# Optimization experiments

Measured on AMD Instinct MI355X. Metric: run time of the kernel, lower is better.

Reference implementation:

```python
import jax, jax.numpy as jnp
import numpy as np

D_MODEL = 2048
D_LATENT = 512


def setup_inputs() -> dict:
    key = jax.random.key(0)
    ks = jax.random.split(key, 6)
    x = jax.random.normal(ks[0], (2, 4096, D_MODEL), dtype=jnp.float32)
    cache = jax.random.normal(ks[1], (2, 4096, D_LATENT), dtype=jnp.float32)
    s = 0.02
    # weights stored (in_features, out_features); equivalent to torch Linear (no bias)
    W_kv = jax.random.normal(ks[2], (D_MODEL, D_LATENT), dtype=jnp.float32) * s
    W_q = jax.random.normal(ks[3], (D_MODEL, D_MODEL), dtype=jnp.float32) * s
    W_lq = jax.random.normal(ks[4], (D_MODEL, D_LATENT), dtype=jnp.float32) * s
    W_o = jax.random.normal(ks[5], (D_LATENT, D_MODEL), dtype=jnp.float32) * s
    return {"x": x, "cache": cache, "W_kv": W_kv, "W_q": W_q, "W_lq": W_lq, "W_o": W_o}


def reference(x, cache, W_kv, W_q, W_lq, W_o):
    # latent compression of inputs: (B, S, d_latent)
    l_kv_new = jnp.einsum('bsd,dl->bsl', x, W_kv)
    # query path: x -> query (d_model) -> latent query (d_latent)
    q = jnp.einsum('bsd,de->bse', x, W_q)
    lq = jnp.einsum('bse,el->bsl', q, W_lq)
    # append to cache: (B, T+S, d_latent)
    l_kv = jnp.concatenate([cache, l_kv_new], axis=1)
    scale = jnp.sqrt(jnp.float32(D_LATENT)).astype(x.dtype)
    # attention in latent space: scores (B, S, T+S)
    scores = jnp.einsum('bsl,btl->bst', lq, l_kv) / scale
    weights = jax.nn.softmax(scores, axis=-1)
    ctx = jnp.einsum('bst,btl->bsl', weights, l_kv)
    out = jnp.einsum('bsl,ld->bsd', ctx, W_o)
    return out, l_kv
```

## Files before the change

kernel.cpp:

```cpp
#include <hip/hip_runtime.h>
#include <hip/hip_bf16.h>
#include <math.h>


typedef _Float16 f16x8 __attribute__((ext_vector_type(8)));
typedef _Float16 f16x4 __attribute__((ext_vector_type(4)));
typedef float    f32x4 __attribute__((ext_vector_type(4)));
typedef float    f32x8 __attribute__((ext_vector_type(8)));


__global__ __launch_bounds__(256) void k_cvt(const float* __restrict__ in,
                                             _Float16* __restrict__ out, int n4) {
  int i = blockIdx.x * blockDim.x + threadIdx.x;
  int st = gridDim.x * blockDim.x;
  for (; i < n4; i += st) {
    f32x4 v = reinterpret_cast<const f32x4*>(in)[i];
    reinterpret_cast<f16x4*>(out)[i] = __builtin_convertvector(v, f16x4);
  }
}

__global__ __launch_bounds__(256) void k_cache(const float* __restrict__ cache,
                                               float* __restrict__ lkv_f32,
                                               _Float16* __restrict__ lkv16, int n4) {
  int i = blockIdx.x * blockDim.x + threadIdx.x;
  int st = gridDim.x * blockDim.x;
  for (; i < n4; i += st) {
    f32x4 v = reinterpret_cast<const f32x4*>(cache)[i];
    int e = i << 2;
    int b = e >> 21;
    int dst = e + (b << 21);
    *reinterpret_cast<f32x4*>(lkv_f32 + dst) = v;
    *reinterpret_cast<f16x4*>(lkv16 + dst) = __builtin_convertvector(v, f16x4);
  }
}

__global__ __launch_bounds__(256) void k_tc(const float* __restrict__ in,
                                            _Float16* __restrict__ out, int R, int C) {
  __shared__ float t[32][33];
  const int c0 = blockIdx.x << 5, r0 = blockIdx.y << 5;
  const int tid = threadIdx.x;
  {
    int r = tid >> 3, c4 = (tid & 7) << 2;
    f32x4 v = *reinterpret_cast<const f32x4*>(&in[(long)(r0 + r) * C + c0 + c4]);
    t[r][c4] = v[0]; t[r][c4 + 1] = v[1]; t[r][c4 + 2] = v[2]; t[r][c4 + 3] = v[3];
  }
  __syncthreads();
  {
    int c = tid >> 3, r4 = (tid & 7) << 2;
    f16x4 o = {(_Float16)t[r4][c], (_Float16)t[r4 + 1][c],
               (_Float16)t[r4 + 2][c], (_Float16)t[r4 + 3][c]};
    *reinterpret_cast<f16x4*>(&out[(long)(c0 + c) * R + r0 + r4]) = o;
  }
}

__global__ __launch_bounds__(256) void k_tb(const _Float16* __restrict__ in,
                                            _Float16* __restrict__ out, int R, int C) {
  __shared__ _Float16 t[32][36];
  const int c0 = blockIdx.x << 5, r0 = blockIdx.y << 5;
  const int tid = threadIdx.x;
  {
    int r = tid >> 3, c4 = (tid & 7) << 2;
    f16x4 v = *reinterpret_cast<const f16x4*>(&in[(long)(r0 + r) * C + c0 + c4]);
    t[r][c4] = v[0]; t[r][c4 + 1] = v[1]; t[r][c4 + 2] = v[2]; t[r][c4 + 3] = v[3];
  }
  __syncthreads();
  {
    int c = tid >> 3, r4 = (tid & 7) << 2;
    f16x4 o = {t[r4][c], t[r4 + 1][c], t[r4 + 2][c], t[r4 + 3][c]};
    *reinterpret_cast<f16x4*>(&out[(long)(c0 + c) * R + r0 + r4]) = o;
  }
}

template <int CMODE>
__global__ __launch_bounds__(256) void k_gemm(const _Float16* __restrict__ A,
                                              const _Float16* __restrict__ B,
                                              float* __restrict__ Cf,
                                              _Float16* __restrict__ Ch,
                                              int M, int N, int K, int lda, int ldb,
                                              float cscale) {
  if constexpr (CMODE == 4) {
    const long z = blockIdx.z;
    A += z * K;
    B += z * K;
    Cf += z * (long)M * N;
  }
  __shared__ alignas(16) _Float16 As[128 * 64];
  __shared__ alignas(16) _Float16 Bs[128 * 64];
  const int tid = threadIdx.x;
  const int lane = tid & 63;
  const int w = tid >> 6;
  const int wr = ((w >> 1) & 1) << 6, wc = (w & 1) << 6;
  const int bm = blockIdx.x << 7, bn = blockIdx.y << 7;
  const int g = lane >> 4, ln15 = lane & 15;

  f32x4 acc[4][4] = {};

  const int srowl = lane >> 3;
  const int skcol = (lane & 7) << 3;
  const int wofs = (srowl << 6) + (((lane & 7) ^ srowl) << 3);

  f16x8 ra[4], rb[4];
  auto loadregs = [&](int k0) {
#pragma unroll
    for (int i = 0; i < 4; ++i) {
      int ch = (w << 2) + i;
      int row = (ch << 3) + srowl;
      ra[i] = *reinterpret_cast<const f16x8*>(&A[(long)(bm + row) * lda + k0 + skcol]);
      rb[i] = *reinterpret_cast<const f16x8*>(&B[(long)(bn + row) * ldb + k0 + skcol]);
    }
  };
  loadregs(0);
  const int nk = K >> 6;
  for (int kt = 0; kt < nk; ++kt) {
    __syncthreads();
#pragma unroll
    for (int i = 0; i < 4; ++i) {
      int ch = (w << 2) + i;
      *reinterpret_cast<f16x8*>(&As[(ch << 9) + wofs]) = ra[i];
      *reinterpret_cast<f16x8*>(&Bs[(ch << 9) + wofs]) = rb[i];
    }
    __syncthreads();
    if (kt + 1 < nk) loadregs((kt + 1) << 6);
#pragma unroll
    for (int ks = 0; ks < 2; ++ks) {
      f16x8 af[4], bf[4];
#pragma unroll
      for (int i = 0; i < 4; ++i) {
        const int arow = wr + (i << 4) + ln15;
        const int brow = wc + (i << 4) + ln15;
        const int inner = (((ks << 5) + (g << 3)) ^ ((ln15 & 7) << 3));
        af[i] = *reinterpret_cast<const f16x8*>(&As[arow * 64 + inner]);
        bf[i] = *reinterpret_cast<const f16x8*>(&Bs[brow * 64 + inner]);
      }
#pragma unroll
      for (int i = 0; i < 4; ++i)
#pragma unroll
        for (int j = 0; j < 4; ++j)
          acc[i][j] = __builtin_amdgcn_mfma_f32_16x16x32_f16(af[i], bf[j], acc[i][j], 0, 0, 0);
    }
  }
#pragma unroll
  for (int i = 0; i < 4; ++i) {
    const int row = bm + wr + (i << 4) + (g << 2);
#pragma unroll
    for (int j = 0; j < 4; ++j) {
      const int col = bn + wc + (j << 4) + ln15;
#pragma unroll
      for (int r = 0; r < 4; ++r) {
        float v = acc[i][j][r];
        long orow = row + r;
        if constexpr (CMODE == 2) {
          long m2 = ((orow >> 12) << 13) + 4096 + (orow & 4095);
          Cf[m2 * 512 + col] = v;
          Ch[m2 * 512 + col] = (_Float16)v;
        } else if constexpr (CMODE == 1) {
          Ch[orow * N + col] = (_Float16)v;
        } else if constexpr (CMODE == 3) {
          Ch[orow * N + col] = (_Float16)(v * cscale);
        } else {
          Cf[orow * N + col] = v;
        }
      }
    }
  }
}

__global__ __launch_bounds__(256) void k_red4(const float* __restrict__ p,
                                              _Float16* __restrict__ o,
                                              int n4, float scale) {
  const f32x4* pv = reinterpret_cast<const f32x4*>(p);
  int i = blockIdx.x * blockDim.x + threadIdx.x;
  int st = gridDim.x * blockDim.x;
  for (; i < n4; i += st) {
    f32x4 a = pv[i] + pv[i + n4] + pv[i + 2 * n4] + pv[i + 3 * n4];
    a *= scale;
    reinterpret_cast<f16x4*>(o)[i] = __builtin_convertvector(a, f16x4);
  }
}

__global__ __launch_bounds__(256) void k_smax(_Float16* __restrict__ S) {
  const int tid = threadIdx.x;
  _Float16* row = S + ((long)blockIdx.x << 13);
  __shared__ float red[4];
  f16x8 v[4];
#pragma unroll
  for (int c = 0; c < 4; ++c)
    v[c] = *reinterpret_cast<const f16x8*>(row + (c << 11) + (tid << 3));
  float mx = -1e30f;
#pragma unroll
  for (int c = 0; c < 4; ++c) {
    f32x8 f = __builtin_convertvector(v[c], f32x8);
#pragma unroll
    for (int j = 0; j < 8; ++j) mx = fmaxf(mx, f[j]);
  }
#pragma unroll
  for (int o = 32; o > 0; o >>= 1) mx = fmaxf(mx, __shfl_xor(mx, o));
  if ((tid & 63) == 0) red[tid >> 6] = mx;
  __syncthreads();
  mx = fmaxf(fmaxf(red[0], red[1]), fmaxf(red[2], red[3]));
  float sum = 0.f;
  f32x8 p0, p1, p2, p3;
  {
    f32x8 f;
#define SMAX_EXP(PC, CI)                                         \
    f = __builtin_convertvector(v[CI], f32x8);                   \
    _Pragma("unroll")                                            \
    for (int j = 0; j < 8; ++j) { PC[j] = __expf(f[j] - mx); sum += PC[j]; }
    SMAX_EXP(p0, 0) SMAX_EXP(p1, 1) SMAX_EXP(p2, 2) SMAX_EXP(p3, 3)
#undef SMAX_EXP
  }
#pragma unroll
  for (int o = 32; o > 0; o >>= 1) sum += __shfl_xor(sum, o);
  __syncthreads();
  if ((tid & 63) == 0) red[tid >> 6] = sum;
  __syncthreads();
  const float inv = 1.f / (red[0] + red[1] + red[2] + red[3]);
  *reinterpret_cast<f16x8*>(row + (0 << 11) + (tid << 3)) = __builtin_convertvector(p0 * inv, f16x8);
  *reinterpret_cast<f16x8*>(row + (1 << 11) + (tid << 3)) = __builtin_convertvector(p1 * inv, f16x8);
  *reinterpret_cast<f16x8*>(row + (2 << 11) + (tid << 3)) = __builtin_convertvector(p2 * inv, f16x8);
  *reinterpret_cast<f16x8*>(row + (3 << 11) + (tid << 3)) = __builtin_convertvector(p3 * inv, f16x8);
}


extern "C" void kernel_launch(void* const* d_in, const int* in_sizes, int n_in,
                              void* d_out, int out_size, void* d_ws, size_t ws_size,
                              hipStream_t stream) {
  const float* x     = (const float*)d_in[0];
  const float* cache = (const float*)d_in[1];
  const float* W_kv  = (const float*)d_in[2];
  const float* W_q   = (const float*)d_in[3];
  const float* W_lq  = (const float*)d_in[4];
  const float* W_o   = (const float*)d_in[5];

  float* out     = (float*)d_out;
  float* lkv_out = out + (size_t)8192 * 2048;

  _Float16* base16 = (_Float16*)d_out;
  _Float16* x16    = base16;
  _Float16* lq16   = base16 + 16777216;
  _Float16* Wq16   = base16 + 20971520;
  _Float16* WlqT   = base16 + 25165824;
  _Float16* WcombT = base16 + 26214400;
  _Float16* WkvT   = base16 + 27262976;
  _Float16* lkvT16 = base16 + 20971520;
  float*    PVp    = (float*)d_out;

  _Float16* lkv16 = (_Float16*)d_ws;
  _Float16* ctx   = lkv16 + 8388608;
  _Float16* WoT   = ctx + 4194304;
  _Float16* Sbuf  = WoT + 1048576;
  float*    Wcp   = (float*)Sbuf;

  const size_t sbase = 27262976;
  int CR = 1024;
  if (ws_size >= sbase + (size_t)4096 * 8192 * 2) CR = 4096;
  else if (ws_size >= sbase + (size_t)2048 * 8192 * 2) CR = 2048;

  const float iscale = 0.044194173824159216f;

  k_cvt<<<1024, 256, 0, stream>>>(x, x16, 16777216 / 4);
  k_cache<<<1024, 256, 0, stream>>>(cache, lkv_out, lkv16, 4194304 / 4);
  k_tc<<<dim3(16, 64), 256, 0, stream>>>(W_kv, WkvT, 2048, 512);
  k_cvt<<<1024, 256, 0, stream>>>(W_q, Wq16, 4194304 / 4);
  k_tc<<<dim3(16, 64), 256, 0, stream>>>(W_lq, WlqT, 2048, 512);
  k_tc<<<dim3(64, 16), 256, 0, stream>>>(W_o, WoT, 512, 2048);

  k_gemm<2><<<dim3(64, 4), 256, 0, stream>>>(x16, WkvT, lkv_out, lkv16,
                                             8192, 512, 2048, 2048, 2048, 1.f);
  k_gemm<4><<<dim3(4, 16, 4), 256, 0, stream>>>(WlqT, Wq16, Wcp, nullptr,
                                                512, 2048, 512, 2048, 2048, 1.f);
  k_red4<<<1024, 256, 0, stream>>>(Wcp, WcombT, (512 * 2048) / 4, iscale);
  k_gemm<1><<<dim3(64, 4), 256, 0, stream>>>(x16, WcombT, nullptr, lq16,
                                             8192, 512, 2048, 2048, 2048, 1.f);
  k_tb<<<dim3(16, 512), 256, 0, stream>>>(lkv16, lkvT16, 16384, 512);

  for (long r0 = 0; r0 < 8192; r0 += CR) {
    const long b = r0 >> 12;
    k_gemm<1><<<dim3(CR >> 7, 64), 256, 0, stream>>>(
        lq16 + r0 * 512, lkv16 + b * 8192 * 512, nullptr, Sbuf,
        CR, 8192, 512, 512, 512, 1.f);
    k_smax<<<CR, 256, 0, stream>>>(Sbuf);
    k_gemm<4><<<dim3(CR >> 7, 4, 4), 256, 0, stream>>>(
        Sbuf, lkvT16 + b * 8192, PVp, nullptr,
        CR, 512, 2048, 8192, 16384, 1.f);
    k_red4<<<2048, 256, 0, stream>>>(PVp, ctx + r0 * 512, (CR * 512) / 4, 1.f);
  }

  k_gemm<0><<<dim3(64, 16), 256, 0, stream>>>(ctx, WoT, out, nullptr,
                                              8192, 2048, 512, 512, 512, 1.f);
}
```

Baseline: 371.8 us.

## Add 256x256-tile GEMM with direct global-to-LDS loads for scores and output projection

Introduces a new 512-thread GEMM kernel with 256x256 output tiles, double-buffered LDS filled via global_load_lds with XOR swizzling, and explicit waitcnt/barrier scheduling. It replaces the previous 128-tile GEMM for the QK^T scores computation and the final W_o projection. The larger tiles raise arithmetic intensity and the direct-to-LDS loads skip register staging. In exchange it uses 128KB of dynamic LDS per block, which limits occupancy, and it requires M and N to be multiples of 256.

New measurement: 375.7 us. No clear change (+1.1%).

```diff
diff --git a/kernel.cpp b/kernel.cpp
--- a/kernel.cpp
+++ b/kernel.cpp
@@ -7,6 +7,12 @@
 typedef _Float16 f16x4 __attribute__((ext_vector_type(4)));
 typedef float    f32x4 __attribute__((ext_vector_type(4)));
 typedef float    f32x8 __attribute__((ext_vector_type(8)));
+
+__device__ __forceinline__ void gl_lds16(const void* g, void* l) {
+  __builtin_amdgcn_global_load_lds(
+      (const __attribute__((address_space(1))) void*)g,
+      (__attribute__((address_space(3))) void*)l, 16, 0, 0);
+}
 
 
 __global__ __launch_bounds__(256) void k_cvt(const float* __restrict__ in,
@@ -165,6 +171,101 @@
   }
 }
 
+template <int CMODE>
+__global__ __launch_bounds__(512, 2) void k_gemm256(const _Float16* __restrict__ A,
+                                                    const _Float16* __restrict__ B,
+                                                    float* __restrict__ Cf,
+                                                    _Float16* __restrict__ Ch,
+                                                    int M, int N, int K,
+                                                    int lda, int ldb) {
+  extern __shared__ _Float16 sm[];
+  _Float16* As = sm;
+  _Float16* Bs = sm + 32768;
+  const int tid = threadIdx.x;
+  const int lane = tid & 63;
+  const int w = tid >> 6;
+  const int wm = w >> 2, wn = w & 3;
+  const int bm = blockIdx.x << 8, bn = blockIdx.y << 8;
+  const int g = lane >> 4, ln15 = lane & 15;
+
+  f32x4 acc[8][4] = {};
+
+  const int lrow8 = lane >> 3;
+  const int lswz  = ((lane & 7) ^ lrow8) << 3;
+  const _Float16* Ap[4];
+  const _Float16* Bp[4];
+  int loff[4];
+#pragma unroll
+  for (int i = 0; i < 4; ++i) {
+    const int row = (i << 6) + (w << 3) + lrow8;
+    Ap[i] = &A[(long)(bm + row) * lda + lswz];
+    Bp[i] = &B[(long)(bn + row) * ldb + lswz];
+    loff[i] = ((i << 6) + (w << 3)) << 6;
+  }
+
+  auto stage = [&](int buf, int kt) {
+    const int k0 = kt << 6;
+    const int bo = buf << 14;
+#pragma unroll
+    for (int i = 0; i < 4; ++i) {
+      gl_lds16(Ap[i] + k0, &As[bo + loff[i]]);
+      gl_lds16(Bp[i] + k0, &Bs[bo + loff[i]]);
+    }
+  };
+
+  const int nk = K >> 6;
+  stage(0, 0);
+  if (nk > 1) stage(1, 1);
+
+  for (int kt = 0; kt < nk; ++kt) {
+    if (kt + 1 < nk) asm volatile("s_waitcnt vmcnt(8)" ::: "memory");
+    else             asm volatile("s_waitcnt vmcnt(0)" ::: "memory");
+    __builtin_amdgcn_sched_barrier(0);
+    __builtin_amdgcn_s_barrier();
+    const int bo = (kt & 1) << 14;
+#pragma unroll
+    for (int ks = 0; ks < 2; ++ks) {
+      f16x8 af[8], bf[4];
+      const int innersw = ((ks << 5) + (g << 3)) ^ ((ln15 & 7) << 3);
+#pragma unroll
+      for (int i = 0; i < 8; ++i) {
+        const int arow = (wm << 7) + (i << 4) + ln15;
+        af[i] = *reinterpret_cast<const f16x8*>(&As[bo + arow * 64 + innersw]);
+      }
+#pragma unroll
+      for (int j = 0; j < 4; ++j) {
+        const int brow = (wn << 6) + (j << 4) + ln15;
+        bf[j] = *reinterpret_cast<const f16x8*>(&Bs[bo + brow * 64 + innersw]);
+      }
+#pragma unroll
+      for (int i = 0; i < 8; ++i)
+#pragma unroll
+        for (int j = 0; j < 4; ++j)
+          acc[i][j] = __builtin_amdgcn_mfma_f32_16x16x32_f16(af[i], bf[j], acc[i][j], 0, 0, 0);
+    }
+    asm volatile("s_waitcnt lgkmcnt(0)" ::: "memory");
+    __builtin_amdgcn_sched_barrier(0);
+    __builtin_amdgcn_s_barrier();
+    if (kt + 2 < nk) stage(kt & 1, kt + 2);
+  }
+
+#pragma unroll
+  for (int i = 0; i < 8; ++i) {
+    const int row = bm + (wm << 7) + (i << 4) + (g << 2);
+#pragma unroll
+    for (int j = 0; j < 4; ++j) {
+      const int col = bn + (wn << 6) + (j << 4) + ln15;
+#pragma unroll
+      for (int r = 0; r < 4; ++r) {
+        if constexpr (CMODE == 1)
+          Ch[(long)(row + r) * N + col] = (_Float16)acc[i][j][r];
+        else
+          Cf[(long)(row + r) * N + col] = acc[i][j][r];
+      }
+    }
+  }
+}
+
 __global__ __launch_bounds__(256) void k_red4(const float* __restrict__ p,
                                               _Float16* __restrict__ o,
                                               int n4, float scale) {
@@ -258,6 +359,11 @@
 
   const float iscale = 0.044194173824159216f;
 
+  hipFuncSetAttribute((const void*)k_gemm256<1>,
+                      hipFuncAttributeMaxDynamicSharedMemorySize, 131072);
+  hipFuncSetAttribute((const void*)k_gemm256<0>,
+                      hipFuncAttributeMaxDynamicSharedMemorySize, 131072);
+
   k_cvt<<<1024, 256, 0, stream>>>(x, x16, 16777216 / 4);
   k_cache<<<1024, 256, 0, stream>>>(cache, lkv_out, lkv16, 4194304 / 4);
   k_tc<<<dim3(16, 64), 256, 0, stream>>>(W_kv, WkvT, 2048, 512);
@@ -276,9 +382,9 @@
 
   for (long r0 = 0; r0 < 8192; r0 += CR) {
     const long b = r0 >> 12;
-    k_gemm<1><<<dim3(CR >> 7, 64), 256, 0, stream>>>(
+    k_gemm256<1><<<dim3(CR >> 8, 32), 512, 131072, stream>>>(
         lq16 + r0 * 512, lkv16 + b * 8192 * 512, nullptr, Sbuf,
-        CR, 8192, 512, 512, 512, 1.f);
+        CR, 8192, 512, 512, 512);
     k_smax<<<CR, 256, 0, stream>>>(Sbuf);
     k_gemm<4><<<dim3(CR >> 7, 4, 4), 256, 0, stream>>>(
         Sbuf, lkvT16 + b * 8192, PVp, nullptr,
@@ -286,6 +392,6 @@
     k_red4<<<2048, 256, 0, stream>>>(PVp, ctx + r0 * 512, (CR * 512) / 4, 1.f);
   }
 
-  k_gemm<0><<<dim3(64, 16), 256, 0, stream>>>(ctx, WoT, out, nullptr,
-                                              8192, 2048, 512, 512, 512, 1.f);
-}
+  k_gemm256<0><<<dim3(32, 8), 512, 131072, stream>>>(ctx, WoT, out, nullptr,
+                                                     8192, 2048, 512, 512, 512);
+}
```
